# Kernel optimization log

Hardware: AMD Instinct MI355X
Metric: run time of the kernel (lower is better)

## Reference

```python
import jax, jax.numpy as jnp
import numpy as np

B, A, DIN, HID, HEADS, NOUT, K = 256, 64, 64, 128, 4, 2, 7
N = B * A                      # 16384 nodes
C = HID                        # per-head dim == out_channels (module quirk)
SCALE = (HID // HEADS) ** -0.5 # 1/sqrt(32), as in the module


def _xavier(k, shape):
    fan_out, fan_in = shape
    lim = (6.0 / (fan_in + fan_out)) ** 0.5
    return jax.random.uniform(k, shape, jnp.float32, -lim, lim)


def setup_inputs() -> dict:
    key = jax.random.key(0)
    ks = jax.random.split(key, 24)
    x = jax.random.normal(ks[0], (N, DIN), jnp.float32)
    pos_b = jax.random.uniform(ks[1], (B, A, 2), jnp.float32) * 10.0  # [B,A,2]
    pos = pos_b.reshape(N, 2)

    # kNN graph per environment (replicates torch.cdist + topk smallest, drop self)
    d = jnp.linalg.norm(pos_b[:, :, None, :] - pos_b[:, None, :, :], axis=-1)  # [B,A,A]
    _, idx = jax.lax.top_k(-d, K + 1)
    nb = idx[..., 1:]                                   # [B,A,K] neighbor ids
    offs = (jnp.arange(B) * A)[:, None, None]
    src = jnp.broadcast_to(jnp.arange(A)[None, :, None], (B, A, K)) + offs
    dst = nb + offs
    loops = jnp.arange(N)
    edge_index = jnp.stack([
        jnp.concatenate([src.reshape(-1), loops]),
        jnp.concatenate([dst.reshape(-1), loops]),
    ]).astype(jnp.int32)                                # [2, E], E = B*A*K + N

    inp = {"x": x, "pos": pos, "edge_index": edge_index}
    inp["l0_Wq"] = _xavier(ks[2], (HEADS * C, 2))
    inp["l0_Wk"] = _xavier(ks[3], (HEADS * C, 2))
    inp["l0_Wv"] = _xavier(ks[4], (HEADS * C, DIN))
    inp["l0_Wo"] = _xavier(ks[5], (HID, HEADS * C))
    inp["l0_bo"] = jnp.zeros((HID,), jnp.float32)
    inp["l1_Wq"] = _xavier(ks[6], (HEADS * C, 2))
    inp["l1_Wk"] = _xavier(ks[7], (HEADS * C, 2))
    inp["l1_Wv"] = _xavier(ks[8], (HEADS * C, HID))
    inp["l1_Wo"] = _xavier(ks[9], (HID, HEADS * C))
    inp["l1_bo"] = jnp.zeros((HID,), jnp.float32)
    inp["W1"] = _xavier(ks[10], (256, HID))
    inp["b1"] = jnp.zeros((256,), jnp.float32)
    inp["W2"] = _xavier(ks[11], (256, 256))
    inp["b2"] = jnp.zeros((256,), jnp.float32)
    inp["W3"] = _xavier(ks[12], (NOUT, 256))
    inp["b3"] = jnp.zeros((NOUT,), jnp.float32)
    return inp


def _gat(x, pos, src, dst, Wq, Wk, Wv, Wo, bo):
    # positions -> Q/K, features -> V (position-aware attention)
    q = (pos @ Wq.T).reshape(N, HEADS, C)
    k = (pos @ Wk.T).reshape(N, HEADS, C)
    v = (x @ Wv.T).reshape(N, HEADS, C)
    # per-edge logits, segment softmax over incoming edges of dst
    alpha = jnp.einsum('ehc,ehc->eh', q[dst], k[src]) * SCALE        # [E,H]
    amax = jax.ops.segment_max(alpha, dst, num_segments=N)           # [N,H]
    ex = jnp.exp(alpha - amax[dst])
    a = ex / jax.ops.segment_sum(ex, dst, num_segments=N)[dst]
    msg = v[src] * a[..., None]                                      # [E,H,C]
    agg = jax.ops.segment_sum(msg, dst, num_segments=N)              # [N,H,C]
    return agg.reshape(N, HEADS * C) @ Wo.T + bo


def reference(x, pos, edge_index,
              l0_Wq, l0_Wk, l0_Wv, l0_Wo, l0_bo,
              l1_Wq, l1_Wk, l1_Wv, l1_Wo, l1_bo,
              W1, b1, W2, b2, W3, b3):
    src, dst = edge_index[0], edge_index[1]
    h = jnp.tanh(_gat(x, pos, src, dst, l0_Wq, l0_Wk, l0_Wv, l0_Wo, l0_bo))
    h = jnp.tanh(_gat(h, pos, src, dst, l1_Wq, l1_Wk, l1_Wv, l1_Wo, l1_bo))
    h = jax.nn.relu(h @ W1.T + b1)
    h = jax.nn.relu(h @ W2.T + b2)
    out = h @ W3.T + b3
    return out.reshape(B, A, NOUT)
```

## Files before the change

### kernel.cpp

```cpp
#include <hip/hip_runtime.h>
#include <hip/hip_bf16.h>
#include <cstddef>
#include <math.h>

#define N_NODES 16384
#define DIN 64
#define HID 128
#define SCALE_F 0.17677669529663687f

using bf16x8 = __attribute__((ext_vector_type(8))) short;
using f32x4  = __attribute__((ext_vector_type(4))) float;

__device__ __forceinline__ ushort f2b(float x) {
  __hip_bfloat16 h = __float2bfloat16(x);
  return *(ushort*)&h;
}
__device__ __forceinline__ float b2f(ushort u) {
  __hip_bfloat16 h = *(__hip_bfloat16*)&u;
  return __bfloat162float(h);
}
__device__ __forceinline__ void split1(float x, ushort& h, ushort& l) {
  h = f2b(x);
  l = f2b(x - b2f(h));
}
__device__ __forceinline__ void split3(float x, ushort& a, ushort& b, ushort& c) {
  a = f2b(x);
  float r1 = x - b2f(a);
  b = f2b(r1);
  c = f2b(r1 - b2f(b));
}

#define MFMA(d, A, B) d = __builtin_amdgcn_mfma_f32_16x16x32_bf16(A, B, d, 0, 0, 0)


__global__ __launch_bounds__(256) void prep_all_kernel(
    const float* __restrict__ Wq0, const float* __restrict__ Wk0,
    const float* __restrict__ Wq1, const float* __restrict__ Wk1,
    float* __restrict__ G,
    const float* __restrict__ Wv0, const float* __restrict__ Wo0,
    ushort* __restrict__ M0a, ushort* __restrict__ M0b, ushort* __restrict__ M0c,
    const float* __restrict__ Wv1, const float* __restrict__ Wo1,
    ushort* __restrict__ M1a, ushort* __restrict__ M1b, ushort* __restrict__ M1c,
    const float* __restrict__ W1, ushort* __restrict__ W1hi, ushort* __restrict__ W1lo,
    const float* __restrict__ W2, ushort* __restrict__ W2hi, ushort* __restrict__ W2lo,
    unsigned long long* __restrict__ out64)
{
  int blk = blockIdx.x, t = threadIdx.x;
  if (blk == 0) {
    if (t >= 32) return;
    int l = t >> 4, h = (t >> 2) & 3, a = (t >> 1) & 1, b = t & 1;
    const float* Wq = l ? Wq1 : Wq0;
    const float* Wk = l ? Wk1 : Wk0;
    float acc = 0.f;
    for (int c = 0; c < 128; c++)
      acc += Wq[(h * 128 + c) * 2 + a] * Wk[(h * 128 + c) * 2 + b];
    G[t] = acc;
  } else if (blk < 385) {
    int D, idx;
    const float *Wv, *Wo;
    ushort *Ma, *Mb, *Mc;
    if (blk < 129) { D = DIN; idx = (blk - 1) * 256 + t; Wv = Wv0; Wo = Wo0; Ma = M0a; Mb = M0b; Mc = M0c; }
    else           { D = HID; idx = (blk - 129) * 256 + t; Wv = Wv1; Wo = Wo1; Ma = M1a; Mb = M1b; Mc = M1c; }
    int K4 = 4 * D;
    int o = idx / K4, hd = idx - o * K4;
    int h = hd / D, d = hd - h * D;
    const float* wv = Wv + (size_t)(h * 128) * D + d;
    const float* wo = Wo + (size_t)o * 512 + h * 128;
    float acc = 0.f;
    for (int c = 0; c < 128; c++)
      acc += wv[(size_t)c * D] * wo[c];
    split3(acc, Ma[idx], Mb[idx], Mc[idx]);
  } else if (blk < 769) {
    int i = (blk - 385) * 256 + t;
    if (i < 256 * 128) split1(W1[i], W1hi[i], W1lo[i]);
    int j = i - 256 * 128;
    if (j >= 0 && j < 256 * 256) split1(W2[j], W2hi[j], W2lo[j]);
  } else {
    int i = (blk - 769) * 256 + t;
    if (i < N_NODES) out64[i] = 0ull;
  }
}


#define PF 136

template <int KD>
__device__ __forceinline__ void gat_layer(
    int wave, int lm, int lq,
    const ushort* sFa, const ushort* sFb, const ushort* sFc,
    const float* psx, const float* psy,
    const float* pdx, const float* pdy,
    const unsigned long long* m64,
    const float* __restrict__ G,
    const ushort* __restrict__ Ma, const ushort* __restrict__ Mb,
    const ushort* __restrict__ Mc,
    f32x4 hacc[4])
{
  const int K4 = 4 * KD;
  const int o = 16 * wave + lm;
#pragma unroll
  for (int i = 0; i < 4; i++) hacc[i] = (f32x4){0.f, 0.f, 0.f, 0.f};

#pragma unroll 1
  for (int h = 0; h < 4; h++) {
    f32x4 y[4];
#pragma unroll
    for (int i = 0; i < 4; i++) y[i] = (f32x4){0.f, 0.f, 0.f, 0.f};
#pragma unroll 1
    for (int kf = 0; kf < KD / 32; kf++) {
      size_t boff = (size_t)o * K4 + h * KD + kf * 32 + lq * 8;
      bf16x8 ma = *(const bf16x8*)&Ma[boff];
      bf16x8 mb = *(const bf16x8*)&Mb[boff];
      bf16x8 mc = *(const bf16x8*)&Mc[boff];
#pragma unroll
      for (int mp = 0; mp < 2; mp++) {
        int f0 = (mp * 32 + lm) * PF + kf * 32 + lq * 8;
        int f1 = (mp * 32 + 16 + lm) * PF + kf * 32 + lq * 8;
        bf16x8 fa0 = *(const bf16x8*)&sFa[f0], fa1 = *(const bf16x8*)&sFa[f1];
        bf16x8 fb0 = *(const bf16x8*)&sFb[f0], fb1 = *(const bf16x8*)&sFb[f1];
        bf16x8 fc0 = *(const bf16x8*)&sFc[f0], fc1 = *(const bf16x8*)&sFc[f1];
        f32x4 y0 = y[mp * 2], y1 = y[mp * 2 + 1];
        MFMA(y0, fa0, ma); MFMA(y1, fa1, ma);
        MFMA(y0, fa0, mb); MFMA(y1, fa1, mb);
        MFMA(y0, fb0, ma); MFMA(y1, fb1, ma);
        MFMA(y0, fa0, mc); MFMA(y1, fa1, mc);
        MFMA(y0, fc0, ma); MFMA(y1, fc1, ma);
        MFMA(y0, fb0, mb); MFMA(y1, fb1, mb);
        y[mp * 2] = y0; y[mp * 2 + 1] = y1;
      }
    }
    bf16x8 Ya[2], Yb[2];
#pragma unroll
    for (int kb = 0; kb < 2; kb++) {
#pragma unroll
      for (int j = 0; j < 8; j++) {
        int sl = ((2 * lq + (j >> 2)) & 3) * 16 + lm;
        float v0 = __shfl(y[2 * kb][j & 3], sl);
        float v1 = __shfl(y[2 * kb + 1][j & 3], sl);
        float v = (lq & 2) ? v1 : v0;
        ushort ua, ub;
        split1(v, ua, ub);
        Ya[kb][j] = (short)ua; Yb[kb][j] = (short)ub;
      }
    }
    float g0 = G[h * 4], g1 = G[h * 4 + 1], g2 = G[h * 4 + 2], g3 = G[h * 4 + 3];
#pragma unroll
    for (int mtd = 0; mtd < 4; mtd++) {
      float a0 = (g0 * pdx[mtd] + g2 * pdy[mtd]) * SCALE_F;
      float a1 = (g1 * pdx[mtd] + g3 * pdy[mtd]) * SCALE_F;
      float sshift = a0 * pdx[mtd] + a1 * pdy[mtd];
      unsigned mb0 = (unsigned)((m64[mtd] >> (8 * lq)) & 0xFF);
      unsigned mb1 = (unsigned)((m64[mtd] >> (32 + 8 * lq)) & 0xFF);
      float e[16];
      float sum = 0.f;
#pragma unroll
      for (int j = 0; j < 8; j++) {
        e[j]     = ((mb0 >> j) & 1) ? __expf(a0 * psx[j] + a1 * psy[j] - sshift) : 0.f;
        e[8 + j] = ((mb1 >> j) & 1) ? __expf(a0 * psx[8 + j] + a1 * psy[8 + j] - sshift) : 0.f;
        sum += e[j] + e[8 + j];
      }
      sum += __shfl_xor(sum, 16);
      sum += __shfl_xor(sum, 32);
      float inv = 1.f / sum;
      bf16x8 Aa[2], Ab[2];
#pragma unroll
      for (int j = 0; j < 8; j++) {
        ushort ua, ub;
        split1(e[j] * inv, ua, ub);
        Aa[0][j] = (short)ua; Ab[0][j] = (short)ub;
        split1(e[8 + j] * inv, ua, ub);
        Aa[1][j] = (short)ua; Ab[1][j] = (short)ub;
      }
#pragma unroll
      for (int kb = 0; kb < 2; kb++) {
        MFMA(hacc[mtd], Aa[kb], Ya[kb]);
        MFMA(hacc[mtd], Aa[kb], Yb[kb]);
        MFMA(hacc[mtd], Ab[kb], Ya[kb]);
        MFMA(hacc[mtd], Ab[kb], Yb[kb]);
      }
    }
  }
}

__global__ __attribute__((amdgpu_flat_work_group_size(512, 512), amdgpu_waves_per_eu(2)))
void fused_gat_kernel(
    const float* __restrict__ x, const float* __restrict__ pos,
    const int* __restrict__ srcp, const int* __restrict__ dstp,
    const float* __restrict__ G,
    const ushort* __restrict__ M0a, const ushort* __restrict__ M0b, const ushort* __restrict__ M0c,
    const ushort* __restrict__ M1a, const ushort* __restrict__ M1b, const ushort* __restrict__ M1c,
    const float* __restrict__ bo0, const float* __restrict__ bo1,
    const ushort* __restrict__ W1hi, const ushort* __restrict__ W1lo, const float* __restrict__ b1,
    const ushort* __restrict__ W2hi, const ushort* __restrict__ W2lo, const float* __restrict__ b2,
    const float* __restrict__ W3, const float* __restrict__ b3,
    float* __restrict__ outp)
{
  __shared__ __align__(16) ushort uBig[32768];
  ushort* sFa = uBig;
  ushort* sFb = uBig + 8704;
  ushort* sFc = uBig + 17408;
  float* pxs = (float*)(uBig + 26112);
  float* pys = (float*)(uBig + 26240);
  unsigned long long* smask = (unsigned long long*)(uBig + 26368);
  ushort* pA = uBig;
  ushort* pB = uBig + 16384;

  int b = blockIdx.x, t = threadIdx.x;
  int wave = t >> 6, lane = t & 63, lm = lane & 15, lq = lane >> 4;

  if (t < 64) {
    pxs[t] = pos[(b * 64 + t) * 2];
    pys[t] = pos[(b * 64 + t) * 2 + 1];
    smask[t] = 1ull << t;
  }
  {
    const float4* gx = (const float4*)(x + (size_t)b * 64 * DIN);
#pragma unroll
    for (int i = 0; i < 2; i++) {
      int idx = t + i * 512;
      float4 v = gx[idx];
      int r = idx >> 4, c = (idx & 15) * 4;
      ushort4 ua, ub, uc;
      split3(v.x, ua.x, ub.x, uc.x); split3(v.y, ua.y, ub.y, uc.y);
      split3(v.z, ua.z, ub.z, uc.z); split3(v.w, ua.w, ub.w, uc.w);
      *(ushort4*)&sFa[r * PF + c] = ua;
      *(ushort4*)&sFb[r * PF + c] = ub;
      *(ushort4*)&sFc[r * PF + c] = uc;
    }
  }
  __syncthreads();
  if (t < 448) {
    int s = srcp[b * 448 + t];
    int d = dstp[b * 448 + t];
    atomicOr(&smask[d & 63], 1ull << (s & 63));
  }
  __syncthreads();
  unsigned long long m64[4];
#pragma unroll
  for (int mtd = 0; mtd < 4; mtd++) m64[mtd] = smask[mtd * 16 + lm];

  float psx[16], psy[16], pdx[4], pdy[4];
#pragma unroll
  for (int j = 0; j < 8; j++) {
    psx[j] = pxs[8 * lq + j];          psy[j] = pys[8 * lq + j];
    psx[8 + j] = pxs[32 + 8 * lq + j]; psy[8 + j] = pys[32 + 8 * lq + j];
  }
#pragma unroll
  for (int mtd = 0; mtd < 4; mtd++) {
    pdx[mtd] = pxs[mtd * 16 + lm];
    pdy[mtd] = pys[mtd * 16 + lm];
  }

  f32x4 hacc[4];
  gat_layer<DIN>(wave, lm, lq, sFa, sFb, sFc, psx, psy, pdx, pdy, m64,
                 G, M0a, M0b, M0c, hacc);
  __syncthreads();
  int o = 16 * wave + lm;
  {
    float bv = bo0[o];
#pragma unroll
    for (int mtd = 0; mtd < 4; mtd++)
#pragma unroll
      for (int r = 0; r < 4; r++) {
        int dst = mtd * 16 + lq * 4 + r;
        ushort ua, ub, uc;
        split3(tanhf(hacc[mtd][r] + bv), ua, ub, uc);
        sFa[dst * PF + o] = ua;
        sFb[dst * PF + o] = ub;
        sFc[dst * PF + o] = uc;
      }
  }
  __syncthreads();
  gat_layer<HID>(wave, lm, lq, sFa, sFb, sFc, psx, psy, pdx, pdy, m64,
                 G + 16, M1a, M1b, M1c, hacc);
  float h2v[4][4];
  {
    float bv = bo1[o];
#pragma unroll
    for (int mtd = 0; mtd < 4; mtd++)
#pragma unroll
      for (int r = 0; r < 4; r++)
        h2v[mtd][r] = tanhf(hacc[mtd][r] + bv);
  }
  __syncthreads();
#pragma unroll
  for (int mtd = 0; mtd < 4; mtd++)
#pragma unroll
    for (int r = 0; r < 4; r++) {
      int dst = mtd * 16 + lq * 4 + r;
      ushort hh, ll;
      split1(h2v[mtd][r], hh, ll);
      sFa[dst * PF + o] = hh;
      sFb[dst * PF + o] = ll;
    }
  __syncthreads();
  f32x4 y1[2][4];
#pragma unroll
  for (int ti = 0; ti < 2; ti++)
#pragma unroll
    for (int mtd = 0; mtd < 4; mtd++) y1[ti][mtd] = (f32x4){0.f, 0.f, 0.f, 0.f};
#pragma unroll 1
  for (int kf = 0; kf < 4; kf++) {
    int ko = kf * 32 + lq * 8;
    bf16x8 bh0 = *(const bf16x8*)&W1hi[(size_t)(32 * wave + lm) * 128 + ko];
    bf16x8 bl0 = *(const bf16x8*)&W1lo[(size_t)(32 * wave + lm) * 128 + ko];
    bf16x8 bh1 = *(const bf16x8*)&W1hi[(size_t)(32 * wave + 16 + lm) * 128 + ko];
    bf16x8 bl1 = *(const bf16x8*)&W1lo[(size_t)(32 * wave + 16 + lm) * 128 + ko];
#pragma unroll
    for (int mtd = 0; mtd < 4; mtd++) {
      bf16x8 ah = *(const bf16x8*)&sFa[(mtd * 16 + lm) * PF + ko];
      bf16x8 al = *(const bf16x8*)&sFb[(mtd * 16 + lm) * PF + ko];
      MFMA(y1[0][mtd], ah, bh0);
      MFMA(y1[0][mtd], ah, bl0);
      MFMA(y1[0][mtd], al, bh0);
      MFMA(y1[1][mtd], ah, bh1);
      MFMA(y1[1][mtd], ah, bl1);
      MFMA(y1[1][mtd], al, bh1);
    }
  }
  __syncthreads();
#pragma unroll
  for (int ti = 0; ti < 2; ti++) {
    int col = 32 * wave + ti * 16 + lm;
    float bv = b1[col];
#pragma unroll
    for (int mtd = 0; mtd < 4; mtd++)
#pragma unroll
      for (int r = 0; r < 4; r++) {
        int row = mtd * 16 + lq * 4 + r;
        float v = fmaxf(y1[ti][mtd][r] + bv, 0.f);
        ushort hh, ll;
        split1(v, hh, ll);
        int cc = col ^ ((row & 15) << 3);
        pA[row * 256 + cc] = hh;
        pB[row * 256 + cc] = ll;
      }
  }
  __syncthreads();
  f32x4 y2[2][4];
#pragma unroll
  for (int ti = 0; ti < 2; ti++)
#pragma unroll
    for (int mtd = 0; mtd < 4; mtd++) y2[ti][mtd] = (f32x4){0.f, 0.f, 0.f, 0.f};
#pragma unroll 1
  for (int kf = 0; kf < 8; kf++) {
    int ko = kf * 32 + lq * 8;
    bf16x8 bh0 = *(const bf16x8*)&W2hi[(size_t)(32 * wave + lm) * 256 + ko];
    bf16x8 bl0 = *(const bf16x8*)&W2lo[(size_t)(32 * wave + lm) * 256 + ko];
    bf16x8 bh1 = *(const bf16x8*)&W2hi[(size_t)(32 * wave + 16 + lm) * 256 + ko];
    bf16x8 bl1 = *(const bf16x8*)&W2lo[(size_t)(32 * wave + 16 + lm) * 256 + ko];
#pragma unroll
    for (int mtd = 0; mtd < 4; mtd++) {
      int row = mtd * 16 + lm;
      int cc = ko ^ ((row & 15) << 3);
      bf16x8 ah = *(const bf16x8*)&pA[row * 256 + cc];
      bf16x8 al = *(const bf16x8*)&pB[row * 256 + cc];
      MFMA(y2[0][mtd], ah, bh0);
      MFMA(y2[0][mtd], ah, bl0);
      MFMA(y2[0][mtd], al, bh0);
      MFMA(y2[1][mtd], ah, bh1);
      MFMA(y2[1][mtd], ah, bl1);
      MFMA(y2[1][mtd], al, bh1);
    }
  }
  {
    int c0 = 32 * wave + lm, c1 = c0 + 16;
    float w300 = W3[c0], w301 = W3[c1];
    float w310 = W3[256 + c0], w311 = W3[256 + c1];
    float b20 = b2[c0], b21 = b2[c1];
    float bb0 = (wave == 0) ? b3[0] : 0.f;
    float bb1 = (wave == 0) ? b3[1] : 0.f;
#pragma unroll
    for (int mtd = 0; mtd < 4; mtd++)
#pragma unroll
      for (int r = 0; r < 4; r++) {
        float va = fmaxf(y2[0][mtd][r] + b20, 0.f);
        float vb = fmaxf(y2[1][mtd][r] + b21, 0.f);
        float s0 = va * w300 + vb * w301;
        float s1 = va * w310 + vb * w311;
        s0 += __shfl_xor(s0, 1); s0 += __shfl_xor(s0, 2);
        s0 += __shfl_xor(s0, 4); s0 += __shfl_xor(s0, 8);
        s1 += __shfl_xor(s1, 1); s1 += __shfl_xor(s1, 2);
        s1 += __shfl_xor(s1, 4); s1 += __shfl_xor(s1, 8);
        if (lm == 0) {
          int row = b * 64 + mtd * 16 + lq * 4 + r;
          atomicAdd(&outp[row * 2 + 0], s0 + bb0);
          atomicAdd(&outp[row * 2 + 1], s1 + bb1);
        }
      }
  }
}


extern "C" void kernel_launch(void* const* d_in, const int* in_sizes, int n_in,
                              void* d_out, int out_size, void* d_ws, size_t ws_size,
                              hipStream_t stream) {
  const float* x     = (const float*)d_in[0];
  const float* pos   = (const float*)d_in[1];
  const int*   ei    = (const int*)d_in[2];
  const float* l0_Wq = (const float*)d_in[3];
  const float* l0_Wk = (const float*)d_in[4];
  const float* l0_Wv = (const float*)d_in[5];
  const float* l0_Wo = (const float*)d_in[6];
  const float* l0_bo = (const float*)d_in[7];
  const float* l1_Wq = (const float*)d_in[8];
  const float* l1_Wk = (const float*)d_in[9];
  const float* l1_Wv = (const float*)d_in[10];
  const float* l1_Wo = (const float*)d_in[11];
  const float* l1_bo = (const float*)d_in[12];
  const float* W1    = (const float*)d_in[13];
  const float* b1    = (const float*)d_in[14];
  const float* W2    = (const float*)d_in[15];
  const float* b2    = (const float*)d_in[16];
  const float* W3    = (const float*)d_in[17];
  const float* b3    = (const float*)d_in[18];
  float* outp = (float*)d_out;

  int E = in_sizes[2] / 2;
  const int* srcp = ei;
  const int* dstp = ei + E;

  char* base = (char*)d_ws;
  size_t off = 0;
  auto alloc = [&](size_t bytes) -> void* {
    void* p = base + off;
    off = (off + bytes + 255) & ~(size_t)255;
    return p;
  };
  float*  G   = (float*)alloc(32 * sizeof(float));
  ushort* M0a = (ushort*)alloc((size_t)128 * 256 * 2);
  ushort* M0b = (ushort*)alloc((size_t)128 * 256 * 2);
  ushort* M0c = (ushort*)alloc((size_t)128 * 256 * 2);
  ushort* M1a = (ushort*)alloc((size_t)128 * 512 * 2);
  ushort* M1b = (ushort*)alloc((size_t)128 * 512 * 2);
  ushort* M1c = (ushort*)alloc((size_t)128 * 512 * 2);
  ushort* W1hi = (ushort*)alloc((size_t)256 * 128 * 2);
  ushort* W1lo = (ushort*)alloc((size_t)256 * 128 * 2);
  ushort* W2hi = (ushort*)alloc((size_t)256 * 256 * 2);
  ushort* W2lo = (ushort*)alloc((size_t)256 * 256 * 2);

  prep_all_kernel<<<833, 256, 0, stream>>>(
      l0_Wq, l0_Wk, l1_Wq, l1_Wk, G,
      l0_Wv, l0_Wo, M0a, M0b, M0c,
      l1_Wv, l1_Wo, M1a, M1b, M1c,
      W1, W1hi, W1lo, W2, W2hi, W2lo,
      (unsigned long long*)outp);

  fused_gat_kernel<<<N_NODES / 64, 512, 0, stream>>>(
      x, pos, srcp, dstp, G, M0a, M0b, M0c, M1a, M1b, M1c, l0_bo, l1_bo,
      W1hi, W1lo, b1, W2hi, W2lo, b2, W3, b3, outp);

  (void)n_in; (void)out_size; (void)ws_size;
}
```

Baseline: 170.8 us.

## Compute attention weight fragments once per block and share via LDS

Previously every wave recomputed the full 64x64 softmax attention fragments (exp, masking, normalisation, bf16 split) for all heads and destination tiles, redundantly across the 8 waves. Now each wave computes a distinct slice (one dst tile and two heads), writes the bf16 hi/lo fragments to a new LDS region, and after a barrier all waves read them for the MFMA aggregation. LDS usage grows from 64KB to about 116KB and the MLP staging buffers are moved to that region. This lets one __syncthreads before the layer-1 MLP epilogue be dropped. The extra LDS may limit occupancy and adds a barrier per GAT layer.

```diff
diff --git a/kernel.cpp b/kernel.cpp
--- a/kernel.cpp
+++ b/kernel.cpp
@@ -84,10 +84,14 @@
 
 #define PF 136
 
+#define AFRAG_OFF 26624
+#define LDS_USHORTS 59392
+
 template <int KD>
 __device__ __forceinline__ void gat_layer(
-    int wave, int lm, int lq,
+    int wave, int lane, int lm, int lq,
     const ushort* sFa, const ushort* sFb, const ushort* sFc,
+    ushort* aA,
     const float* psx, const float* psy,
     const float* pdx, const float* pdy,
     const unsigned long long* m64,
@@ -96,6 +100,48 @@
     const ushort* __restrict__ Mc,
     f32x4 hacc[4])
 {
+  {
+    int wm = wave & 3;
+    float pdxm = (wm & 2) ? ((wm & 1) ? pdx[3] : pdx[2]) : ((wm & 1) ? pdx[1] : pdx[0]);
+    float pdym = (wm & 2) ? ((wm & 1) ? pdy[3] : pdy[2]) : ((wm & 1) ? pdy[1] : pdy[0]);
+    unsigned long long mm = (wm & 2) ? ((wm & 1) ? m64[3] : m64[2])
+                                     : ((wm & 1) ? m64[1] : m64[0]);
+    unsigned mb0 = (unsigned)((mm >> (8 * lq)) & 0xFF);
+    unsigned mb1 = (unsigned)((mm >> (32 + 8 * lq)) & 0xFF);
+#pragma unroll
+    for (int pi = 0; pi < 2; pi++) {
+      int h = (wave >> 2) + 2 * pi;
+      float g0 = G[h * 4], g1 = G[h * 4 + 1], g2 = G[h * 4 + 2], g3 = G[h * 4 + 3];
+      float a0 = (g0 * pdxm + g2 * pdym) * SCALE_F;
+      float a1 = (g1 * pdxm + g3 * pdym) * SCALE_F;
+      float sshift = a0 * pdxm + a1 * pdym;
+      float e[16];
+      float sum = 0.f;
+#pragma unroll
+      for (int j = 0; j < 8; j++) {
+        e[j]     = ((mb0 >> j) & 1) ? __expf(a0 * psx[j] + a1 * psy[j] - sshift) : 0.f;
+        e[8 + j] = ((mb1 >> j) & 1) ? __expf(a0 * psx[8 + j] + a1 * psy[8 + j] - sshift) : 0.f;
+        sum += e[j] + e[8 + j];
+      }
+      sum += __shfl_xor(sum, 16);
+      sum += __shfl_xor(sum, 32);
+      float inv = 1.f / sum;
+      bf16x8 Aa0, Aa1, Ab0, Ab1;
+#pragma unroll
+      for (int j = 0; j < 8; j++) {
+        ushort ua, ub;
+        split1(e[j] * inv, ua, ub);     Aa0[j] = (short)ua; Ab0[j] = (short)ub;
+        split1(e[8 + j] * inv, ua, ub); Aa1[j] = (short)ua; Ab1[j] = (short)ub;
+      }
+      int sbase = (h * 4 + wm) * 2048 + lane * 8;
+      *(bf16x8*)&aA[sbase]        = Aa0;
+      *(bf16x8*)&aA[sbase + 512]  = Aa1;
+      *(bf16x8*)&aA[sbase + 1024] = Ab0;
+      *(bf16x8*)&aA[sbase + 1536] = Ab1;
+    }
+  }
+  __syncthreads();
+
   const int K4 = 4 * KD;
   const int o = 16 * wave + lm;
 #pragma unroll
@@ -143,41 +189,21 @@
         Ya[kb][j] = (short)ua; Yb[kb][j] = (short)ub;
       }
     }
-    float g0 = G[h * 4], g1 = G[h * 4 + 1], g2 = G[h * 4 + 2], g3 = G[h * 4 + 3];
 #pragma unroll
     for (int mtd = 0; mtd < 4; mtd++) {
-      float a0 = (g0 * pdx[mtd] + g2 * pdy[mtd]) * SCALE_F;
-      float a1 = (g1 * pdx[mtd] + g3 * pdy[mtd]) * SCALE_F;
-      float sshift = a0 * pdx[mtd] + a1 * pdy[mtd];
-      unsigned mb0 = (unsigned)((m64[mtd] >> (8 * lq)) & 0xFF);
-      unsigned mb1 = (unsigned)((m64[mtd] >> (32 + 8 * lq)) & 0xFF);
-      float e[16];
-      float sum = 0.f;
-#pragma unroll
-      for (int j = 0; j < 8; j++) {
-        e[j]     = ((mb0 >> j) & 1) ? __expf(a0 * psx[j] + a1 * psy[j] - sshift) : 0.f;
-        e[8 + j] = ((mb1 >> j) & 1) ? __expf(a0 * psx[8 + j] + a1 * psy[8 + j] - sshift) : 0.f;
-        sum += e[j] + e[8 + j];
-      }
-      sum += __shfl_xor(sum, 16);
-      sum += __shfl_xor(sum, 32);
-      float inv = 1.f / sum;
-      bf16x8 Aa[2], Ab[2];
-#pragma unroll
-      for (int j = 0; j < 8; j++) {
-        ushort ua, ub;
-        split1(e[j] * inv, ua, ub);
-        Aa[0][j] = (short)ua; Ab[0][j] = (short)ub;
-        split1(e[8 + j] * inv, ua, ub);
-        Aa[1][j] = (short)ua; Ab[1][j] = (short)ub;
-      }
-#pragma unroll
-      for (int kb = 0; kb < 2; kb++) {
-        MFMA(hacc[mtd], Aa[kb], Ya[kb]);
-        MFMA(hacc[mtd], Aa[kb], Yb[kb]);
-        MFMA(hacc[mtd], Ab[kb], Ya[kb]);
-        MFMA(hacc[mtd], Ab[kb], Yb[kb]);
-      }
+      int abase = (h * 4 + mtd) * 2048 + lane * 8;
+      bf16x8 Aa0 = *(const bf16x8*)&aA[abase];
+      bf16x8 Aa1 = *(const bf16x8*)&aA[abase + 512];
+      bf16x8 Ab0 = *(const bf16x8*)&aA[abase + 1024];
+      bf16x8 Ab1 = *(const bf16x8*)&aA[abase + 1536];
+      MFMA(hacc[mtd], Aa0, Ya[0]);
+      MFMA(hacc[mtd], Aa0, Yb[0]);
+      MFMA(hacc[mtd], Ab0, Ya[0]);
+      MFMA(hacc[mtd], Ab0, Yb[0]);
+      MFMA(hacc[mtd], Aa1, Ya[1]);
+      MFMA(hacc[mtd], Aa1, Yb[1]);
+      MFMA(hacc[mtd], Ab1, Ya[1]);
+      MFMA(hacc[mtd], Ab1, Yb[1]);
     }
   }
 }
@@ -195,15 +221,16 @@
     const float* __restrict__ W3, const float* __restrict__ b3,
     float* __restrict__ outp)
 {
-  __shared__ __align__(16) ushort uBig[32768];
+  __shared__ __align__(16) ushort uBig[LDS_USHORTS];
   ushort* sFa = uBig;
   ushort* sFb = uBig + 8704;
   ushort* sFc = uBig + 17408;
   float* pxs = (float*)(uBig + 26112);
   float* pys = (float*)(uBig + 26240);
   unsigned long long* smask = (unsigned long long*)(uBig + 26368);
-  ushort* pA = uBig;
-  ushort* pB = uBig + 16384;
+  ushort* aA = uBig + AFRAG_OFF;
+  ushort* pA = uBig + AFRAG_OFF;
+  ushort* pB = uBig + AFRAG_OFF + 16384;
 
   int b = blockIdx.x, t = threadIdx.x;
   int wave = t >> 6, lane = t & 63, lm = lane & 15, lq = lane >> 4;
@@ -252,7 +279,7 @@
   }
 
   f32x4 hacc[4];
-  gat_layer<DIN>(wave, lm, lq, sFa, sFb, sFc, psx, psy, pdx, pdy, m64,
+  gat_layer<DIN>(wave, lane, lm, lq, sFa, sFb, sFc, aA, psx, psy, pdx, pdy, m64,
                  G, M0a, M0b, M0c, hacc);
   __syncthreads();
   int o = 16 * wave + lm;
@@ -271,7 +298,7 @@
       }
   }
   __syncthreads();
-  gat_layer<HID>(wave, lm, lq, sFa, sFb, sFc, psx, psy, pdx, pdy, m64,
+  gat_layer<HID>(wave, lane, lm, lq, sFa, sFb, sFc, aA, psx, psy, pdx, pdy, m64,
                  G + 16, M1a, M1b, M1c, hacc);
   float h2v[4][4];
   {
@@ -318,7 +345,6 @@
       MFMA(y1[1][mtd], al, bh1);
     }
   }
-  __syncthreads();
 #pragma unroll
   for (int ti = 0; ti < 2; ti++) {
     int col = 32 * wave + ti * 16 + lm;
```

Result: faster. 160.0 us (-6.4%).
